# Kernel tuning notes

Hardware: AMD Instinct MI355X
Metric: run time of the kernel (lower is better)

## Reference

```python
import jax, jax.numpy as jnp
import numpy as np

B, S, DIN, DOUT = 2, 2048, 4096, 4096


def setup_inputs() -> dict:
    key = jax.random.key(0)
    k1, k2 = jax.random.split(key)
    x = jax.random.normal(k1, (B, S, DIN), dtype=jnp.float32)
    weight = jax.random.normal(k2, (DOUT, DIN), dtype=jnp.float32) * 0.02
    # xnor init for row scaling pattern
    mean = weight.mean(-1, keepdims=True)                      # [DOUT,1]
    scale = jnp.abs(weight - mean).mean(-1, keepdims=True)     # [DOUT,1]
    wscale = scale
    wbias = mean
    return {"x": x, "weight": weight, "wscale": wscale, "wbias": wbias}


def reference(x, weight, wscale, wbias):
    # STE binarization: forward = sign(weight) (grad handled in bwd module)
    w_bin = jnp.sign(weight)
    w = wscale * w_bin + wbias                                 # [DOUT, DIN]
    # F.linear(x, w): x @ w.T, no bias
    out = jnp.einsum('bsk,nk->bsn', x, w)
    return out
```

## Files before the change

### kernel.cpp

```cpp
#include <hip/hip_runtime.h>
#include <stdint.h>


#define MDIM 4096
#define NDIM 4096
#define KDIM 4096

typedef int int4v  __attribute__((ext_vector_type(4)));
typedef int int16v __attribute__((ext_vector_type(16)));

__device__ __forceinline__ int pack4_rn(float a, float b, float c, float d, float inv) {
  int ia = __float2int_rn(a * inv) & 0xff;
  int ib = __float2int_rn(b * inv) & 0xff;
  int ic = __float2int_rn(c * inv) & 0xff;
  int id = __float2int_rn(d * inv) & 0xff;
  return ia | (ib << 8) | (ic << 16) | (id << 24);
}

__device__ __forceinline__ int sgn8(float v) {
  return (v > 0.f) ? 1 : ((v < 0.f) ? 0xff : 0);
}

#define PREP_XB 1024
#define PREP_WB 1024
__global__ __launch_bounds__(256) void prep_kernel(
    const float* __restrict__ x, const float* __restrict__ w,
    char* __restrict__ xq, char* __restrict__ wsg,
    float* __restrict__ xscale, float* __restrict__ sumx) {
  const int b = blockIdx.x;
  const int tid = threadIdx.x;
  const int lane = tid & 63, wv = tid >> 6;
  if (b < PREP_XB) {
    const int row = b * 4 + wv;
    const float4* xr = (const float4*)(x + (size_t)row * KDIM);
    float4 v[16];
    float s = 0.f, amax = 0.f;
#pragma unroll
    for (int u = 0; u < 16; ++u) {
      v[u] = xr[u * 64 + lane];
      s += v[u].x + v[u].y + v[u].z + v[u].w;
      amax = fmaxf(amax, fmaxf(fmaxf(fabsf(v[u].x), fabsf(v[u].y)),
                               fmaxf(fabsf(v[u].z), fabsf(v[u].w))));
    }
#pragma unroll
    for (int off = 32; off > 0; off >>= 1) {
      s += __shfl_xor(s, off, 64);
      amax = fmaxf(amax, __shfl_xor(amax, off, 64));
    }
    if (lane == 0) {
      sumx[row] = s;
      xscale[row] = amax * (1.f / 127.f);
    }
    const float inv = (amax > 0.f) ? 127.f / amax : 0.f;
    int* xo = (int*)(xq + (size_t)row * KDIM);
#pragma unroll
    for (int u = 0; u < 16; ++u)
      xo[u * 64 + lane] = pack4_rn(v[u].x, v[u].y, v[u].z, v[u].w, inv);
  } else {
    const float4* wr = (const float4*)w;
    int* wo = (int*)wsg;
    const size_t i0 = (size_t)(b - PREP_XB) * 256 + tid;
    const size_t stride = (size_t)PREP_WB * 256;
#pragma unroll
    for (int u = 0; u < 16; ++u) {
      size_t i = i0 + (size_t)u * stride;
      float4 vv = wr[i];
      wo[i] = sgn8(vv.x) | (sgn8(vv.y) << 8) | (sgn8(vv.z) << 16) | (sgn8(vv.w) << 24);
    }
  }
}

__global__ __launch_bounds__(512, 4) void gemm_bin_i8_cohab(
    const char* __restrict__ A, const char* __restrict__ Bs,
    const float* __restrict__ wscale, const float* __restrict__ wbias,
    const float* __restrict__ xscale, const float* __restrict__ sumx,
    float* __restrict__ C) {
  __shared__ __align__(16) char sm[49152];

  const int bid = blockIdx.x;
  const int xcd = bid & 7, loc = bid >> 3;
  const int bm = (xcd >> 1) * 4 + (loc >> 4);
  const int bn = (xcd & 1) * 16 + (loc & 15);
  const int tm0 = bm * 256, tn0 = bn * 128;
  const int tid = threadIdx.x;
  const int lane = tid & 63, wave = tid >> 6;
  const int col32 = lane & 31, hl = lane >> 5;
  const int wr = wave >> 1, wc = wave & 1;

  int16v acc[2][2];
#pragma unroll
  for (int mi = 0; mi < 2; ++mi)
#pragma unroll
    for (int nj = 0; nj < 2; ++nj)
#pragma unroll
      for (int r = 0; r < 16; ++r) acc[mi][nj][r] = 0;

  int4v af[4], bq[4];

  const int swc = (col32 >> 1) & 3;
  int aBase[2], bBase[2];
#pragma unroll
  for (int ks2 = 0; ks2 < 2; ++ks2) {
    aBase[ks2] = (wr * 64 + col32) * 64 + (((ks2 * 2 + hl) ^ swc) & 3) * 16;
    bBase[ks2] = 32768 + (wc * 64 + col32) * 64 + (((ks2 * 2 + hl) ^ swc) & 3) * 16;
  }

  const int uA0 = tid, uA1 = tid + 512, uB = tid;
  const int rA0 = uA0 >> 2, rA1 = uA1 >> 2, rB = uB >> 2;
  const int offsA0 = rA0 * KDIM + (((uA0 & 3) ^ ((rA0 >> 1) & 3))) * 16;
  const int offsA1 = rA1 * KDIM + (((uA1 & 3) ^ ((rA1 >> 1) & 3))) * 16;
  const int offsB  = rB * KDIM + (((uB & 3) ^ ((rB >> 1) & 3))) * 16;
  const char* Abase = A + (size_t)tm0 * KDIM;
  const char* Bbase = Bs + (size_t)tn0 * KDIM;
  const int ldt = tid * 16;

#define STAGE(BUF, KOFS)                                                          \
  do {                                                                            \
    const int sa_ = (BUF) * 16384;                                                \
    const int sb_ = 32768 + (BUF) * 8192;                                         \
    __builtin_amdgcn_global_load_lds(                                             \
        (const __attribute__((address_space(1))) void*)(Abase + offsA0 + (KOFS)), \
        (__attribute__((address_space(3))) void*)(sm + sa_ + ldt), 16, 0, 0);     \
    __builtin_amdgcn_global_load_lds(                                             \
        (const __attribute__((address_space(1))) void*)(Abase + offsA1 + (KOFS)), \
        (__attribute__((address_space(3))) void*)(sm + sa_ + 8192 + ldt), 16, 0, 0);\
    __builtin_amdgcn_global_load_lds(                                             \
        (const __attribute__((address_space(1))) void*)(Bbase + offsB + (KOFS)),  \
        (__attribute__((address_space(3))) void*)(sm + sb_ + ldt), 16, 0, 0);     \
  } while (0)

#define DSRD(BUF)                                                                 \
  do {                                                                            \
    const int sa_ = (BUF) * 16384;                                                \
    const int sb_ = (BUF) * 8192;                                                 \
    af[0] = *(const int4v*)(sm + sa_ + aBase[0]);                                 \
    af[1] = *(const int4v*)(sm + sa_ + aBase[0] + 2048);                          \
    bq[0] = *(const int4v*)(sm + sb_ + bBase[0]);                                 \
    bq[1] = *(const int4v*)(sm + sb_ + bBase[0] + 2048);                          \
    af[2] = *(const int4v*)(sm + sa_ + aBase[1]);                                 \
    af[3] = *(const int4v*)(sm + sa_ + aBase[1] + 2048);                          \
    bq[2] = *(const int4v*)(sm + sb_ + bBase[1]);                                 \
    bq[3] = *(const int4v*)(sm + sb_ + bBase[1] + 2048);                          \
  } while (0)

#define MFMA4(KS2)                                                                \
  do {                                                                            \
    __builtin_amdgcn_s_setprio(1);                                                \
    _Pragma("unroll") for (int mi_ = 0; mi_ < 2; ++mi_)                           \
        _Pragma("unroll") for (int nj_ = 0; nj_ < 2; ++nj_)                       \
            acc[mi_][nj_] = __builtin_amdgcn_mfma_i32_32x32x32_i8(                \
                af[(KS2) * 2 + mi_], bq[(KS2) * 2 + nj_], acc[mi_][nj_], 0, 0, 0);\
    __builtin_amdgcn_s_setprio(0);                                                \
  } while (0)

#define WAITL(N)                                                                  \
  do {                                                                            \
    asm volatile("s_waitcnt lgkmcnt(" #N ")" ::: "memory");                       \
    __builtin_amdgcn_sched_barrier(0);                                            \
  } while (0)

#define CKV0 asm volatile("s_waitcnt vmcnt(0)\n\ts_barrier" ::: "memory")

#define PHASE(BUF, STAGEOP, ENDSYNC)                                              \
  do {                                                                            \
    STAGEOP;                                                                      \
    DSRD(BUF);                                                                    \
    WAITL(4);                                                                     \
    MFMA4(0);                                                                     \
    WAITL(0);                                                                     \
    MFMA4(1);                                                                     \
    ENDSYNC;                                                                      \
  } while (0)

  STAGE(0, 0);
  CKV0;

#pragma unroll 1
  for (int t = 0; t < 62; t += 2) {
    PHASE(0, STAGE(1, (t + 1) * 64), CKV0);
    PHASE(1, STAGE(0, (t + 2) * 64), CKV0);
  }
  PHASE(0, STAGE(1, 63 * 64), CKV0);
  PHASE(1, (void)0, (void)0);

#undef PHASE
#undef CKV0
#undef WAITL
#undef MFMA4
#undef DSRD
#undef STAGE

  float wsv[2], wbv[2];
#pragma unroll
  for (int nj = 0; nj < 2; ++nj) {
    int n = tn0 + wc * 64 + nj * 32 + col32;
    wsv[nj] = wscale[n];
    wbv[nj] = wbias[n];
  }
#pragma unroll
  for (int mi = 0; mi < 2; ++mi) {
#pragma unroll
    for (int reg = 0; reg < 16; ++reg) {
      int m = tm0 + wr * 64 + mi * 32 + (reg & 3) + 8 * (reg >> 2) + 4 * hl;
      float xs = xscale[m];
      float sx = sumx[m];
      float* crow = C + (size_t)m * NDIM + tn0 + wc * 64 + col32;
#pragma unroll
      for (int nj = 0; nj < 2; ++nj)
        crow[nj * 32] = wsv[nj] * xs * (float)acc[mi][nj][reg] + wbv[nj] * sx;
    }
  }
}

extern "C" void kernel_launch(void* const* d_in, const int* in_sizes, int n_in,
                              void* d_out, int out_size, void* d_ws, size_t ws_size,
                              hipStream_t stream) {
  const float* x      = (const float*)d_in[0];
  const float* weight = (const float*)d_in[1];
  const float* wscale = (const float*)d_in[2];
  const float* wbias  = (const float*)d_in[3];
  float* out = (float*)d_out;

  char* xq  = (char*)d_ws;
  char* wsg = xq + (size_t)MDIM * KDIM;
  float* xscale = (float*)(wsg + (size_t)NDIM * KDIM);
  float* sumx   = xscale + MDIM;

  prep_kernel<<<PREP_XB + PREP_WB, 256, 0, stream>>>(
      x, weight, xq, wsg, xscale, sumx);
  gemm_bin_i8_cohab<<<(MDIM / 256) * (NDIM / 128), 512, 0, stream>>>(
      xq, wsg, wscale, wbias, xscale, sumx, out);
}
```

Before: 245.3 us.

## Enlarge int8 GEMM tile to 256x256 with K=128 stages and 16x16x64 MFMA

The binarized int8 GEMM moves from 256x128 output tiles with 64-wide K steps and 32x32x32 MFMAs to 256x256 tiles with 128-wide K steps, 16x16x64 MFMAs, and 128KB of double-buffered LDS with an 8-way XOR swizzle. Each wave now computes a 128x64 sub-tile, and global-to-LDS staging is split into four quarter-phases interleaved with compute. The aim is more data reuse per byte loaded and fewer barriers per unit of K. The cost is 256 blocks instead of 512, lower occupancy (2 blocks per CU by launch bounds, and LDS usage likely allows only one), more barriers within each tile, and higher register pressure.

```diff
diff --git a/kernel.cpp b/kernel.cpp
--- a/kernel.cpp
+++ b/kernel.cpp
@@ -6,8 +6,7 @@
 #define NDIM 4096
 #define KDIM 4096
 
-typedef int int4v  __attribute__((ext_vector_type(4)));
-typedef int int16v __attribute__((ext_vector_type(16)));
+typedef int int4v __attribute__((ext_vector_type(4)));
 
 __device__ __forceinline__ int pack4_rn(float a, float b, float c, float d, float inv) {
   int ia = __float2int_rn(a * inv) & 0xff;
@@ -70,144 +69,149 @@
   }
 }
 
-__global__ __launch_bounds__(512, 4) void gemm_bin_i8_cohab(
+__global__ __launch_bounds__(512, 2) void gemm_bin_i8_r128(
     const char* __restrict__ A, const char* __restrict__ Bs,
     const float* __restrict__ wscale, const float* __restrict__ wbias,
     const float* __restrict__ xscale, const float* __restrict__ sumx,
     float* __restrict__ C) {
-  __shared__ __align__(16) char sm[49152];
+  __shared__ __align__(16) char sm[131072];
 
   const int bid = blockIdx.x;
   const int xcd = bid & 7, loc = bid >> 3;
-  const int bm = (xcd >> 1) * 4 + (loc >> 4);
-  const int bn = (xcd & 1) * 16 + (loc & 15);
-  const int tm0 = bm * 256, tn0 = bn * 128;
+  const int bm = (xcd >> 1) * 4 + (loc >> 3);
+  const int bn = (xcd & 1) * 8 + (loc & 7);
+  const int tm0 = bm * 256, tn0 = bn * 256;
   const int tid = threadIdx.x;
   const int lane = tid & 63, wave = tid >> 6;
-  const int col32 = lane & 31, hl = lane >> 5;
-  const int wr = wave >> 1, wc = wave & 1;
-
-  int16v acc[2][2];
-#pragma unroll
-  for (int mi = 0; mi < 2; ++mi)
-#pragma unroll
-    for (int nj = 0; nj < 2; ++nj)
-#pragma unroll
-      for (int r = 0; r < 16; ++r) acc[mi][nj][r] = 0;
+  const int l15 = lane & 15, q4 = lane >> 4, l7 = lane & 7;
+  const int wr = wave >> 2, wc = wave & 3;
+
+  int4v acc[8][4];
+#pragma unroll
+  for (int fr = 0; fr < 8; ++fr)
+#pragma unroll
+    for (int fc = 0; fc < 4; ++fc) acc[fr][fc] = (int4v){0, 0, 0, 0};
 
   int4v af[4], bq[4];
 
-  const int swc = (col32 >> 1) & 3;
-  int aBase[2], bBase[2];
-#pragma unroll
-  for (int ks2 = 0; ks2 < 2; ++ks2) {
-    aBase[ks2] = (wr * 64 + col32) * 64 + (((ks2 * 2 + hl) ^ swc) & 3) * 16;
-    bBase[ks2] = 32768 + (wc * 64 + col32) * 64 + (((ks2 * 2 + hl) ^ swc) & 3) * 16;
-  }
-
-  const int uA0 = tid, uA1 = tid + 512, uB = tid;
-  const int rA0 = uA0 >> 2, rA1 = uA1 >> 2, rB = uB >> 2;
-  const int offsA0 = rA0 * KDIM + (((uA0 & 3) ^ ((rA0 >> 1) & 3))) * 16;
-  const int offsA1 = rA1 * KDIM + (((uA1 & 3) ^ ((rA1 >> 1) & 3))) * 16;
-  const int offsB  = rB * KDIM + (((uB & 3) ^ ((rB >> 1) & 3))) * 16;
-  const char* Abase = A + (size_t)tm0 * KDIM;
-  const char* Bbase = Bs + (size_t)tn0 * KDIM;
-  const int ldt = tid * 16;
-
-#define STAGE(BUF, KOFS)                                                          \
-  do {                                                                            \
-    const int sa_ = (BUF) * 16384;                                                \
-    const int sb_ = 32768 + (BUF) * 8192;                                         \
-    __builtin_amdgcn_global_load_lds(                                             \
-        (const __attribute__((address_space(1))) void*)(Abase + offsA0 + (KOFS)), \
-        (__attribute__((address_space(3))) void*)(sm + sa_ + ldt), 16, 0, 0);     \
-    __builtin_amdgcn_global_load_lds(                                             \
-        (const __attribute__((address_space(1))) void*)(Abase + offsA1 + (KOFS)), \
-        (__attribute__((address_space(3))) void*)(sm + sa_ + 8192 + ldt), 16, 0, 0);\
-    __builtin_amdgcn_global_load_lds(                                             \
-        (const __attribute__((address_space(1))) void*)(Bbase + offsB + (KOFS)),  \
-        (__attribute__((address_space(3))) void*)(sm + sb_ + ldt), 16, 0, 0);     \
-  } while (0)
-
-#define DSRD(BUF)                                                                 \
-  do {                                                                            \
-    const int sa_ = (BUF) * 16384;                                                \
-    const int sb_ = (BUF) * 8192;                                                 \
-    af[0] = *(const int4v*)(sm + sa_ + aBase[0]);                                 \
-    af[1] = *(const int4v*)(sm + sa_ + aBase[0] + 2048);                          \
-    bq[0] = *(const int4v*)(sm + sb_ + bBase[0]);                                 \
-    bq[1] = *(const int4v*)(sm + sb_ + bBase[0] + 2048);                          \
-    af[2] = *(const int4v*)(sm + sa_ + aBase[1]);                                 \
-    af[3] = *(const int4v*)(sm + sa_ + aBase[1] + 2048);                          \
-    bq[2] = *(const int4v*)(sm + sb_ + bBase[1]);                                 \
-    bq[3] = *(const int4v*)(sm + sb_ + bBase[1] + 2048);                          \
-  } while (0)
-
-#define MFMA4(KS2)                                                                \
-  do {                                                                            \
+  int aAddr[2], bAddr[2];
+#pragma unroll
+  for (int kh = 0; kh < 2; ++kh) {
+    aAddr[kh] = (wr * 128 + l15) * 128 + (((kh * 4 + q4) ^ l7) & 7) * 16;
+    bAddr[kh] = 65536 + (wc * 64 + l15) * 128 + (((kh * 4 + q4) ^ l7) & 7) * 16;
+  }
+
+  const int u0 = tid, u1 = tid + 512;
+  const int gOff0 = (u0 >> 3) * KDIM + (((u0 & 7) ^ ((u0 >> 3) & 7))) * 16;
+  const int gOff1 = (u1 >> 3) * KDIM + (((u1 & 7) ^ ((u1 >> 3) & 7))) * 16;
+  const int ld0 = tid * 16, ld1 = 8192 + tid * 16;
+  const char* Ab = A + (size_t)tm0 * KDIM;
+  const char* Bb = Bs + (size_t)tn0 * KDIM;
+
+#define STAGE_A(BUF, RHALF, KOFS)                                                 \
+  do {                                                                            \
+    const char* g_ = Ab + (RHALF) * 128 * KDIM + (KOFS);                          \
+    const int d_ = (BUF) * 32768 + (RHALF) * 16384;                               \
+    __builtin_amdgcn_global_load_lds(                                             \
+        (const __attribute__((address_space(1))) void*)(g_ + gOff0),              \
+        (__attribute__((address_space(3))) void*)(sm + d_ + ld0), 16, 0, 0);      \
+    __builtin_amdgcn_global_load_lds(                                             \
+        (const __attribute__((address_space(1))) void*)(g_ + gOff1),              \
+        (__attribute__((address_space(3))) void*)(sm + d_ + ld1), 16, 0, 0);      \
+  } while (0)
+
+#define STAGE_B(BUF, RHALF, KOFS)                                                 \
+  do {                                                                            \
+    const char* g_ = Bb + (RHALF) * 128 * KDIM + (KOFS);                          \
+    const int d_ = 65536 + (BUF) * 32768 + (RHALF) * 16384;                       \
+    __builtin_amdgcn_global_load_lds(                                             \
+        (const __attribute__((address_space(1))) void*)(g_ + gOff0),              \
+        (__attribute__((address_space(3))) void*)(sm + d_ + ld0), 16, 0, 0);      \
+    __builtin_amdgcn_global_load_lds(                                             \
+        (const __attribute__((address_space(1))) void*)(g_ + gOff1),              \
+        (__attribute__((address_space(3))) void*)(sm + d_ + ld1), 16, 0, 0);      \
+  } while (0)
+
+#define BARO __builtin_amdgcn_s_barrier()
+#define LG0                                                                       \
+  do {                                                                            \
+    asm volatile("s_waitcnt lgkmcnt(0)" ::: "memory");                            \
+    __builtin_amdgcn_sched_barrier(0);                                            \
+  } while (0)
+#define CKV0 asm volatile("s_waitcnt vmcnt(0)\n\ts_barrier" ::: "memory")
+
+#define PH(BUF, KH, RH, LOADB, STAGEOP, ENDSYNC)                                  \
+  do {                                                                            \
+    _Pragma("unroll") for (int i_ = 0; i_ < 4; ++i_)                              \
+        af[i_] = *(const int4v*)(sm + (BUF) * 32768 + aAddr[KH] +                 \
+                                 ((RH) * 4 + i_) * 2048);                         \
+    if (LOADB) {                                                                  \
+      _Pragma("unroll") for (int j_ = 0; j_ < 4; ++j_)                            \
+          bq[j_] = *(const int4v*)(sm + (BUF) * 32768 + bAddr[KH] + j_ * 2048);   \
+    }                                                                             \
+    STAGEOP;                                                                      \
+    BARO;                                                                         \
+    LG0;                                                                          \
     __builtin_amdgcn_s_setprio(1);                                                \
-    _Pragma("unroll") for (int mi_ = 0; mi_ < 2; ++mi_)                           \
-        _Pragma("unroll") for (int nj_ = 0; nj_ < 2; ++nj_)                       \
-            acc[mi_][nj_] = __builtin_amdgcn_mfma_i32_32x32x32_i8(                \
-                af[(KS2) * 2 + mi_], bq[(KS2) * 2 + nj_], acc[mi_][nj_], 0, 0, 0);\
+    _Pragma("unroll") for (int i_ = 0; i_ < 4; ++i_)                              \
+        _Pragma("unroll") for (int j_ = 0; j_ < 4; ++j_)                          \
+            acc[(RH) * 4 + i_][j_] = __builtin_amdgcn_mfma_i32_16x16x64_i8(       \
+                af[i_], bq[j_], acc[(RH) * 4 + i_][j_], 0, 0, 0);                 \
     __builtin_amdgcn_s_setprio(0);                                                \
-  } while (0)
-
-#define WAITL(N)                                                                  \
-  do {                                                                            \
-    asm volatile("s_waitcnt lgkmcnt(" #N ")" ::: "memory");                       \
-    __builtin_amdgcn_sched_barrier(0);                                            \
-  } while (0)
-
-#define CKV0 asm volatile("s_waitcnt vmcnt(0)\n\ts_barrier" ::: "memory")
-
-#define PHASE(BUF, STAGEOP, ENDSYNC)                                              \
-  do {                                                                            \
-    STAGEOP;                                                                      \
-    DSRD(BUF);                                                                    \
-    WAITL(4);                                                                     \
-    MFMA4(0);                                                                     \
-    WAITL(0);                                                                     \
-    MFMA4(1);                                                                     \
     ENDSYNC;                                                                      \
   } while (0)
 
-  STAGE(0, 0);
+#define TILE(BUF, TAU)                                                            \
+  do {                                                                            \
+    PH(BUF, 0, 0, 1, STAGE_A((BUF) ^ 1, 0, ((TAU) + 1) * 128), BARO);             \
+    PH(BUF, 0, 1, 0, STAGE_A((BUF) ^ 1, 1, ((TAU) + 1) * 128), BARO);             \
+    PH(BUF, 1, 0, 1, STAGE_B((BUF) ^ 1, 0, ((TAU) + 1) * 128), BARO);             \
+    PH(BUF, 1, 1, 0, STAGE_B((BUF) ^ 1, 1, ((TAU) + 1) * 128), CKV0);             \
+  } while (0)
+
+  STAGE_A(0, 0, 0);
+  STAGE_A(0, 1, 0);
+  STAGE_B(0, 0, 0);
+  STAGE_B(0, 1, 0);
   CKV0;
 
 #pragma unroll 1
-  for (int t = 0; t < 62; t += 2) {
-    PHASE(0, STAGE(1, (t + 1) * 64), CKV0);
-    PHASE(1, STAGE(0, (t + 2) * 64), CKV0);
-  }
-  PHASE(0, STAGE(1, 63 * 64), CKV0);
-  PHASE(1, (void)0, (void)0);
-
-#undef PHASE
+  for (int t = 0; t < 30; t += 2) {
+    TILE(0, t);
+    TILE(1, t + 1);
+  }
+  TILE(0, 30);
+  PH(1, 0, 0, 1, (void)0, BARO);
+  PH(1, 0, 1, 0, (void)0, BARO);
+  PH(1, 1, 0, 1, (void)0, BARO);
+  PH(1, 1, 1, 0, (void)0, (void)0);
+
+#undef TILE
+#undef PH
+#undef BARO
+#undef LG0
 #undef CKV0
-#undef WAITL
-#undef MFMA4
-#undef DSRD
-#undef STAGE
-
-  float wsv[2], wbv[2];
-#pragma unroll
-  for (int nj = 0; nj < 2; ++nj) {
-    int n = tn0 + wc * 64 + nj * 32 + col32;
-    wsv[nj] = wscale[n];
-    wbv[nj] = wbias[n];
-  }
-#pragma unroll
-  for (int mi = 0; mi < 2; ++mi) {
-#pragma unroll
-    for (int reg = 0; reg < 16; ++reg) {
-      int m = tm0 + wr * 64 + mi * 32 + (reg & 3) + 8 * (reg >> 2) + 4 * hl;
+#undef STAGE_A
+#undef STAGE_B
+
+  float wsv[4], wbv[4];
+#pragma unroll
+  for (int fc = 0; fc < 4; ++fc) {
+    int n = tn0 + wc * 64 + fc * 16 + l15;
+    wsv[fc] = wscale[n];
+    wbv[fc] = wbias[n];
+  }
+#pragma unroll
+  for (int fr = 0; fr < 8; ++fr) {
+#pragma unroll
+    for (int reg = 0; reg < 4; ++reg) {
+      int m = tm0 + wr * 128 + fr * 16 + q4 * 4 + reg;
       float xs = xscale[m];
       float sx = sumx[m];
-      float* crow = C + (size_t)m * NDIM + tn0 + wc * 64 + col32;
-#pragma unroll
-      for (int nj = 0; nj < 2; ++nj)
-        crow[nj * 32] = wsv[nj] * xs * (float)acc[mi][nj][reg] + wbv[nj] * sx;
+      float* crow = C + (size_t)m * NDIM + tn0 + wc * 64 + l15;
+#pragma unroll
+      for (int fc = 0; fc < 4; ++fc)
+        crow[fc * 16] = wsv[fc] * xs * (float)acc[fr][fc][reg] + wbv[fc] * sx;
     }
   }
 }
@@ -228,6 +232,6 @@
 
   prep_kernel<<<PREP_XB + PREP_WB, 256, 0, stream>>>(
       x, weight, xq, wsg, xscale, sumx);
-  gemm_bin_i8_cohab<<<(MDIM / 256) * (NDIM / 128), 512, 0, stream>>>(
+  gemm_bin_i8_r128<<<(MDIM / 256) * (NDIM / 256), 512, 0, stream>>>(
       xq, wsg, wscale, wbias, xscale, sumx, out);
 }
```

New measurement: 232.0 us. 1.06x faster.
